# Performance work log

Measured on AMD Instinct MI355X. Metric: run time of the kernel, lower is better.

## Reference

```python
import jax, jax.numpy as jnp
import numpy as np

N_EMBD = 1024
HEAD_SIZE = 64

def setup_inputs() -> dict:
    key = jax.random.key(0)
    kx, kk, kq, kv = jax.random.split(key, 4)
    x = jax.random.normal(kx, (8, 2048, N_EMBD), dtype=jnp.float32)
    scale = 1.0 / np.sqrt(N_EMBD)
    # nn.Linear weights are [out, in]; kaiming-uniform-ish init
    Wk = jax.random.uniform(kk, (HEAD_SIZE, N_EMBD), dtype=jnp.float32, minval=-scale, maxval=scale)
    Wq = jax.random.uniform(kq, (HEAD_SIZE, N_EMBD), dtype=jnp.float32, minval=-scale, maxval=scale)
    Wv = jax.random.uniform(kv, (HEAD_SIZE, N_EMBD), dtype=jnp.float32, minval=-scale, maxval=scale)
    return {"x": x, "Wk": Wk, "Wq": Wq, "Wv": Wv}

def reference(x, Wk, Wq, Wv):
    # x: [B, T, E]; W*: [H, E] (torch Linear layout)
    k = jnp.einsum('bte,he->bth', x, Wk)
    q = jnp.einsum('bte,he->bth', x, Wq)
    v = jnp.einsum('bte,he->bth', x, Wv)
    inv_sqrt_h = 1.0 / np.sqrt(HEAD_SIZE)
    wei = jnp.einsum('bth,bsh->bts', q, k) * inv_sqrt_h  # [B, T, T]
    wei = jax.nn.softmax(wei, axis=-1)
    out = jnp.einsum('bts,bsh->bth', wei, v)  # [B, T, H]
    return out
```

## Files before the change

kernel.cpp:

```cpp
#include <hip/hip_runtime.h>
#include <cstdint>

#define NB 8
#define TS 2048
#define NE 1024
#define HD 64
#define MTOT (NB*TS)

typedef float     f4  __attribute__((ext_vector_type(4)));
typedef short     s8v __attribute__((ext_vector_type(8)));
typedef short     s4v __attribute__((ext_vector_type(4)));
typedef int       i4v __attribute__((ext_vector_type(4)));
typedef _Float16  h8  __attribute__((ext_vector_type(8)));

__device__ __forceinline__ short f2bf(float f) {
  union { float f; uint32_t u; } x; x.f = f;
  return (short)((x.u + 0x7FFFu + ((x.u >> 16) & 1u)) >> 16);
}

__device__ __forceinline__ int pack2(float lo, float hi) {
  union { float f; uint32_t u; } a, b; a.f = lo; b.f = hi;
  return (int)__builtin_amdgcn_perm(b.u + 0x8000u, a.u + 0x8000u, 0x07060302u);
}

__device__ __forceinline__ void gl2lds(const void* gptr, void* lptr) {
  auto g = (const __attribute__((address_space(1))) uint32_t*)gptr;
  auto l = (__attribute__((address_space(3))) uint32_t*)lptr;
  __builtin_amdgcn_global_load_lds(g, l, 16, 0, 0);
}

template <int N>
__device__ __forceinline__ void wait_barrier() {
  asm volatile("s_waitcnt vmcnt(%0) lgkmcnt(0)" :: "n"(N) : "memory");
  __builtin_amdgcn_s_barrier();
}

__global__ __launch_bounds__(256) void wconv_kernel(
    const float* __restrict__ Wk, const float* __restrict__ Wq, const float* __restrict__ Wv,
    short* __restrict__ wb)
{
  const int idx = (blockIdx.x * 256 + threadIdx.x) * 4;
  const int p = idx >> 16;
  const int off = idx & 65535;
  const float* W = (p == 0) ? Wq : (p == 1) ? Wk : Wv;
  const float s = (p == 0) ? 0.18033688011112042f : 1.0f;
  const float4 v = *(const float4*)&W[off];
  s4v h; h[0] = f2bf(v.x*s); h[1] = f2bf(v.y*s); h[2] = f2bf(v.z*s); h[3] = f2bf(v.w*s);
  *(s4v*)&wb[idx] = h;
}

__global__ __launch_bounds__(256) void proj_kernel(
    const float* __restrict__ x, const short* __restrict__ wb,
    short* __restrict__ qo, short* __restrict__ ko, _Float16* __restrict__ vo)
{
  __shared__ float Xs[4][32][64];
  __shared__ short Ws[2][192][64];
  const int tid = threadIdx.x;
  const int wv = tid >> 6, lane = tid & 63, n = lane & 15, quad = lane >> 4;
  const int mg = wv & 1, cg = wv >> 1;
  const int r0 = blockIdx.x * 32;
  const int xrow = lane >> 4, xslot = lane & 15;
  const int wrow = lane >> 3, wslot = lane & 7;

  auto dmaX = [&](int c, int buf) {
#pragma unroll
    for (int u = 0; u < 2; ++u) {
      const int R0 = (wv * 2 + u) * 4;
      const int row = R0 + xrow;
      const int gs = (xslot + row) & 15;
      gl2lds(&x[(size_t)(r0 + row) * NE + c * 64 + gs * 4], &Xs[buf][R0][0]);
    }
  };
  auto dmaW = [&](int c, int buf) {
#pragma unroll
    for (int u = 0; u < 6; ++u) {
      const int C0 = (wv * 6 + u) * 8;
      const int col = C0 + wrow;
      const int gs = (wslot + col) & 7;
      gl2lds(&wb[(size_t)col * NE + c * 64 + gs * 8], &Ws[buf][C0][0]);
    }
  };

  const f4 fz = {0.f, 0.f, 0.f, 0.f};
  f4 acc[6] = {fz, fz, fz, fz, fz, fz};

  auto compute = [&](int bw, int bx) {
    s8v a[2];
    const int row = mg * 16 + n;
#pragma unroll
    for (int kc = 0; kc < 2; ++kc) {
      const int u0 = kc * 8 + quad * 2;
      const float* pr = &Xs[bx][row][0];
      const f4 f0 = *(const f4*)(pr + (((u0    ) - row) & 15) * 4);
      const f4 f1 = *(const f4*)(pr + (((u0 + 1) - row) & 15) * 4);
      i4v ai;
      ai[0] = pack2(f0[0], f0[1]); ai[1] = pack2(f0[2], f0[3]);
      ai[2] = pack2(f1[0], f1[1]); ai[3] = pack2(f1[2], f1[3]);
      a[kc] = __builtin_bit_cast(s8v, ai);
    }
#pragma unroll
    for (int nf = 0; nf < 6; ++nf) {
      const int col = cg * 96 + nf * 16 + n;
      const s8v b0 = *(const s8v*)&Ws[bw][col][(((0 + quad) - col) & 7) * 8];
      const s8v b1 = *(const s8v*)&Ws[bw][col][(((4 + quad) - col) & 7) * 8];
      acc[nf] = __builtin_amdgcn_mfma_f32_16x16x32_bf16(a[0], b0, acc[nf], 0, 0, 0);
      acc[nf] = __builtin_amdgcn_mfma_f32_16x16x32_bf16(a[1], b1, acc[nf], 0, 0, 0);
    }
  };

  dmaW(0, 0); dmaX(0, 0); dmaX(1, 1); dmaX(2, 2);
  wait_barrier<4>();

  for (int t = 0; t < 16; ++t) {
    if (t <= 14) dmaW(t + 1, (t + 1) & 1);
    if (t <= 12) dmaX(t + 3, (t + 3) & 3);
    compute(t & 1, t & 3);
    if (t <= 12)      wait_barrier<2>();
    else if (t <= 14) wait_barrier<0>();
  }

#pragma unroll
  for (int nf = 0; nf < 6; ++nf) {
    const int gc = cg * 96 + nf * 16;
    const int p = gc >> 6;
    const int rcol = (gc & 63) + n;
#pragma unroll
    for (int i = 0; i < 4; ++i) {
      const int R = r0 + mg * 16 + quad * 4 + i;
      const float av = acc[nf][i];
      if (p == 0)      qo[(size_t)R * HD + rcol] = f2bf(av);
      else if (p == 1) ko[(size_t)R * HD + rcol] = f2bf(av);
      else {
        const int t2 = R & (TS - 1), b = t2 & 31;
        const int pos = (t2 & ~31) | (((b >> 2) & 3) << 3) | (((b >> 4) & 1) << 2) | (b & 3);
        vo[(size_t)(R >> 11) * HD * TS + (size_t)rcol * TS + pos] = (_Float16)av;
      }
    }
  }
}

__global__ __launch_bounds__(512) void attn_kernel(
    const short* __restrict__ q, const short* __restrict__ k,
    const _Float16* __restrict__ vT, float* __restrict__ out)
{
  __shared__ __align__(16) char smem[98304];
  const int tid = threadIdx.x;
  const int wv = tid >> 6, lane = tid & 63, n = lane & 15, quad = lane >> 4;
  const int half = wv >> 2, qw = wv & 3;
  const int batch = blockIdx.x & 7;
  const int qg = blockIdx.x >> 3;
  const int m0 = batch * TS + qg * 64;
  const short*    kb = k  + (size_t)batch * TS * HD;
  const _Float16* vb = vT + (size_t)batch * HD * TS;
  const int drow = lane >> 3, dslot = lane & 7;
  const f4 fz = {0.f, 0.f, 0.f, 0.f};

  auto kbuf = [&](int buf) { return (short*)   (smem +         (half * 3 + buf) * 8192); };
  auto vbuf = [&](int buf) { return (_Float16*)(smem + 49152 + (half * 3 + buf) * 8192); };

  auto dmaKV = [&](int tt, int buf) {
    const int c = half * 16 + tt;
#pragma unroll
    for (int u = 0; u < 2; ++u) {
      const int K0 = (qw * 2 + u) * 8;
      const int key = K0 + drow;
      const int gs = (dslot + key) & 7;
      gl2lds(&kb[(size_t)(c * 64 + key) * HD + gs * 8], kbuf(buf) + K0 * 64);
    }
#pragma unroll
    for (int u = 0; u < 2; ++u) {
      const int D0 = (qw * 2 + u) * 8;
      const int d = D0 + drow;
      const int gs = (dslot + d) & 7;
      gl2lds(&vb[(size_t)d * TS + c * 64 + gs * 8], vbuf(buf) + D0 * 64);
    }
  };

  s8v qf[2];
#pragma unroll
  for (int kc = 0; kc < 2; ++kc)
    qf[kc] = *(const s8v*)&q[(size_t)(m0 + qw * 16 + n) * HD + kc * 32 + quad * 8];

  f4 o[4] = {fz, fz, fz, fz};
  f4 lD = fz;
  h8 ones;
#pragma unroll
  for (int j = 0; j < 8; ++j) ones[j] = (_Float16)1.0f;

  dmaKV(0, 0); dmaKV(1, 1);
  wait_barrier<4>();

  for (int t = 0; t < 16; ++t) {
    const int buf = t % 3;
    if (t <= 13) dmaKV(t + 2, (t + 2) % 3);

    const short*    ks = kbuf(buf);
    const _Float16* vs = vbuf(buf);

    s8v kf[4][2];
#pragma unroll
    for (int f = 0; f < 4; ++f)
#pragma unroll
      for (int kc = 0; kc < 2; ++kc) {
        const int key = f * 16 + n;
        kf[f][kc] = *(const s8v*)&ks[key * 64 + (((kc * 4 + quad) - key) & 7) * 8];
      }

    f4 st[4];
#pragma unroll
    for (int f = 0; f < 4; ++f) {
      st[f] = __builtin_amdgcn_mfma_f32_16x16x32_bf16(kf[f][0], qf[0], fz, 0, 0, 0);
      st[f] = __builtin_amdgcn_mfma_f32_16x16x32_bf16(kf[f][1], qf[1], st[f], 0, 0, 0);
    }

    h8 pa[2];
#pragma unroll
    for (int pr = 0; pr < 2; ++pr)
#pragma unroll
      for (int hf = 0; hf < 2; ++hf)
#pragma unroll
        for (int i = 0; i < 4; ++i)
          pa[pr][hf * 4 + i] = (_Float16)__builtin_amdgcn_exp2f(st[pr * 2 + hf][i]);

#pragma unroll
    for (int pr = 0; pr < 2; ++pr) {
      lD = __builtin_amdgcn_mfma_f32_16x16x32_f16(pa[pr], ones, lD, 0, 0, 0);
#pragma unroll
      for (int g = 0; g < 4; ++g) {
        const int d = g * 16 + n;
        const h8 vf = *(const h8*)&vs[d * 64 + (((pr * 4 + quad) - d) & 7) * 8];
        o[g] = __builtin_amdgcn_mfma_f32_16x16x32_f16(pa[pr], vf, o[g], 0, 0, 0);
      }
    }

    if (t <= 13)      wait_barrier<4>();
    else if (t == 14) wait_barrier<0>();
  }

  __syncthreads();

  float* o_c = (float*)smem;
  float* l_c = (float*)(smem + 36864);
  if (n == 0)
#pragma unroll
    for (int i = 0; i < 4; ++i) l_c[wv * 16 + quad * 4 + i] = lD[i];
#pragma unroll
  for (int g = 0; g < 4; ++g)
#pragma unroll
    for (int i = 0; i < 4; ++i)
      o_c[(wv * 16 + quad * 4 + i) * 68 + g * 16 + n] = o[g][i];
  __syncthreads();

#pragma unroll
  for (int rep = 0; rep < 2; ++rep) {
    const int idx = tid + rep * 512;
    const int qr = idx >> 4, d4 = (idx & 15) * 4;
    const int qw2 = qr >> 4, wr = qr & 15;
    const float L = l_c[qw2 * 16 + wr] + l_c[(qw2 + 4) * 16 + wr];
    const f4 s0 = *(const f4*)&o_c[(qw2 * 16 + wr) * 68 + d4];
    const f4 s1 = *(const f4*)&o_c[((qw2 + 4) * 16 + wr) * 68 + d4];
    f4 r = (s0 + s1);
    const float inv = 1.0f / L;
    r[0] *= inv; r[1] *= inv; r[2] *= inv; r[3] *= inv;
    *(f4*)&out[(size_t)(m0 + qr) * HD + d4] = r;
  }
}

extern "C" void kernel_launch(void* const* d_in, const int* in_sizes, int n_in,
                              void* d_out, int out_size, void* d_ws, size_t ws_size,
                              hipStream_t stream) {
  const float* x  = (const float*)d_in[0];
  const float* Wk = (const float*)d_in[1];
  const float* Wq = (const float*)d_in[2];
  const float* Wv = (const float*)d_in[3];
  float* out = (float*)d_out;

  short* qb = (short*)d_ws;
  short* kb = qb + (size_t)MTOT * HD;
  _Float16* vb = (_Float16*)(kb + (size_t)MTOT * HD);
  short* wb = (short*)(vb + (size_t)NB * HD * TS);

  wconv_kernel<<<192, 256, 0, stream>>>(Wk, Wq, Wv, wb);
  proj_kernel<<<MTOT / 32, 256, 0, stream>>>(x, wb, qb, kb, vb);
  attn_kernel<<<MTOT / 64, 512, 0, stream>>>(qb, kb, vb, out);
}
```

Baseline: 129.5 us.

## Fuse weight conversion, projection and attention into one persistent kernel with grid barriers

Replaces three launches with one 256-block persistent kernel that converts weights, computes the QKV projection, and runs attention. The phases are separated by atomic-counter grid barriers, and a small memset resets the counters each call. Projection and attention tiling are reworked so each block covers 64 rows, using 32-key K/V tiles with a smaller LDS footprint. This removes launch gaps and inter-kernel drains but adds grid-barrier spin cost and relies on all 256 blocks being co-resident.

New measurement: 366.6 us. +183.1%, slower.

```diff
diff --git a/kernel.cpp b/kernel.cpp
--- a/kernel.cpp
+++ b/kernel.cpp
@@ -6,10 +6,10 @@
 #define NE 1024
 #define HD 64
 #define MTOT (NB*TS)
+#define NBLK 256
 
 typedef float     f4  __attribute__((ext_vector_type(4)));
 typedef short     s8v __attribute__((ext_vector_type(8)));
-typedef short     s4v __attribute__((ext_vector_type(4)));
 typedef int       i4v __attribute__((ext_vector_type(4)));
 typedef _Float16  h8  __attribute__((ext_vector_type(8)));
 
@@ -35,234 +35,230 @@
   __builtin_amdgcn_s_barrier();
 }
 
-__global__ __launch_bounds__(256) void wconv_kernel(
-    const float* __restrict__ Wk, const float* __restrict__ Wq, const float* __restrict__ Wv,
-    short* __restrict__ wb)
-{
-  const int idx = (blockIdx.x * 256 + threadIdx.x) * 4;
-  const int p = idx >> 16;
-  const int off = idx & 65535;
-  const float* W = (p == 0) ? Wq : (p == 1) ? Wk : Wv;
-  const float s = (p == 0) ? 0.18033688011112042f : 1.0f;
-  const float4 v = *(const float4*)&W[off];
-  s4v h; h[0] = f2bf(v.x*s); h[1] = f2bf(v.y*s); h[2] = f2bf(v.z*s); h[3] = f2bf(v.w*s);
-  *(s4v*)&wb[idx] = h;
-}
-
-__global__ __launch_bounds__(256) void proj_kernel(
-    const float* __restrict__ x, const short* __restrict__ wb,
-    short* __restrict__ qo, short* __restrict__ ko, _Float16* __restrict__ vo)
-{
-  __shared__ float Xs[4][32][64];
-  __shared__ short Ws[2][192][64];
-  const int tid = threadIdx.x;
-  const int wv = tid >> 6, lane = tid & 63, n = lane & 15, quad = lane >> 4;
-  const int mg = wv & 1, cg = wv >> 1;
-  const int r0 = blockIdx.x * 32;
-  const int xrow = lane >> 4, xslot = lane & 15;
-  const int wrow = lane >> 3, wslot = lane & 7;
-
-  auto dmaX = [&](int c, int buf) {
-#pragma unroll
-    for (int u = 0; u < 2; ++u) {
-      const int R0 = (wv * 2 + u) * 4;
-      const int row = R0 + xrow;
-      const int gs = (xslot + row) & 15;
-      gl2lds(&x[(size_t)(r0 + row) * NE + c * 64 + gs * 4], &Xs[buf][R0][0]);
-    }
-  };
-  auto dmaW = [&](int c, int buf) {
-#pragma unroll
-    for (int u = 0; u < 6; ++u) {
-      const int C0 = (wv * 6 + u) * 8;
-      const int col = C0 + wrow;
-      const int gs = (wslot + col) & 7;
-      gl2lds(&wb[(size_t)col * NE + c * 64 + gs * 8], &Ws[buf][C0][0]);
-    }
-  };
-
-  const f4 fz = {0.f, 0.f, 0.f, 0.f};
-  f4 acc[6] = {fz, fz, fz, fz, fz, fz};
-
-  auto compute = [&](int bw, int bx) {
-    s8v a[2];
-    const int row = mg * 16 + n;
-#pragma unroll
-    for (int kc = 0; kc < 2; ++kc) {
-      const int u0 = kc * 8 + quad * 2;
-      const float* pr = &Xs[bx][row][0];
-      const f4 f0 = *(const f4*)(pr + (((u0    ) - row) & 15) * 4);
-      const f4 f1 = *(const f4*)(pr + (((u0 + 1) - row) & 15) * 4);
-      i4v ai;
-      ai[0] = pack2(f0[0], f0[1]); ai[1] = pack2(f0[2], f0[3]);
-      ai[2] = pack2(f1[0], f1[1]); ai[3] = pack2(f1[2], f1[3]);
-      a[kc] = __builtin_bit_cast(s8v, ai);
-    }
-#pragma unroll
-    for (int nf = 0; nf < 6; ++nf) {
-      const int col = cg * 96 + nf * 16 + n;
-      const s8v b0 = *(const s8v*)&Ws[bw][col][(((0 + quad) - col) & 7) * 8];
-      const s8v b1 = *(const s8v*)&Ws[bw][col][(((4 + quad) - col) & 7) * 8];
-      acc[nf] = __builtin_amdgcn_mfma_f32_16x16x32_bf16(a[0], b0, acc[nf], 0, 0, 0);
-      acc[nf] = __builtin_amdgcn_mfma_f32_16x16x32_bf16(a[1], b1, acc[nf], 0, 0, 0);
-    }
-  };
-
-  dmaW(0, 0); dmaX(0, 0); dmaX(1, 1); dmaX(2, 2);
-  wait_barrier<4>();
-
-  for (int t = 0; t < 16; ++t) {
-    if (t <= 14) dmaW(t + 1, (t + 1) & 1);
-    if (t <= 12) dmaX(t + 3, (t + 3) & 3);
-    compute(t & 1, t & 3);
-    if (t <= 12)      wait_barrier<2>();
-    else if (t <= 14) wait_barrier<0>();
-  }
-
-#pragma unroll
-  for (int nf = 0; nf < 6; ++nf) {
-    const int gc = cg * 96 + nf * 16;
-    const int p = gc >> 6;
-    const int rcol = (gc & 63) + n;
-#pragma unroll
-    for (int i = 0; i < 4; ++i) {
-      const int R = r0 + mg * 16 + quad * 4 + i;
-      const float av = acc[nf][i];
-      if (p == 0)      qo[(size_t)R * HD + rcol] = f2bf(av);
-      else if (p == 1) ko[(size_t)R * HD + rcol] = f2bf(av);
-      else {
-        const int t2 = R & (TS - 1), b = t2 & 31;
-        const int pos = (t2 & ~31) | (((b >> 2) & 3) << 3) | (((b >> 4) & 1) << 2) | (b & 3);
-        vo[(size_t)(R >> 11) * HD * TS + (size_t)rcol * TS + pos] = (_Float16)av;
-      }
-    }
-  }
-}
-
-__global__ __launch_bounds__(512) void attn_kernel(
-    const short* __restrict__ q, const short* __restrict__ k,
-    const _Float16* __restrict__ vT, float* __restrict__ out)
+__device__ __forceinline__ void gridbar(uint32_t* cnt, int id) {
+  __threadfence();
+  __syncthreads();
+  if (threadIdx.x == 0) {
+    __hip_atomic_fetch_add(&cnt[id], 1u, __ATOMIC_RELEASE, __HIP_MEMORY_SCOPE_AGENT);
+    while (__hip_atomic_load(&cnt[id], __ATOMIC_ACQUIRE, __HIP_MEMORY_SCOPE_AGENT) < NBLK)
+      __builtin_amdgcn_s_sleep(8);
+  }
+  __syncthreads();
+  __threadfence();
+}
+
+__global__ __launch_bounds__(512, 2) void fused_kernel(
+    const float* __restrict__ x, const float* __restrict__ Wk,
+    const float* __restrict__ Wq, const float* __restrict__ Wv,
+    short* __restrict__ wb, short* __restrict__ qo, short* __restrict__ ko,
+    _Float16* __restrict__ vo, float* __restrict__ out, uint32_t* cnt)
 {
   __shared__ __align__(16) char smem[98304];
   const int tid = threadIdx.x;
   const int wv = tid >> 6, lane = tid & 63, n = lane & 15, quad = lane >> 4;
-  const int half = wv >> 2, qw = wv & 3;
-  const int batch = blockIdx.x & 7;
-  const int qg = blockIdx.x >> 3;
-  const int m0 = batch * TS + qg * 64;
-  const short*    kb = k  + (size_t)batch * TS * HD;
-  const _Float16* vb = vT + (size_t)batch * HD * TS;
-  const int drow = lane >> 3, dslot = lane & 7;
+  const int blk = blockIdx.x;
   const f4 fz = {0.f, 0.f, 0.f, 0.f};
 
-  auto kbuf = [&](int buf) { return (short*)   (smem +         (half * 3 + buf) * 8192); };
-  auto vbuf = [&](int buf) { return (_Float16*)(smem + 49152 + (half * 3 + buf) * 8192); };
-
-  auto dmaKV = [&](int tt, int buf) {
-    const int c = half * 16 + tt;
-#pragma unroll
-    for (int u = 0; u < 2; ++u) {
-      const int K0 = (qw * 2 + u) * 8;
-      const int key = K0 + drow;
-      const int gs = (dslot + key) & 7;
-      gl2lds(&kb[(size_t)(c * 64 + key) * HD + gs * 8], kbuf(buf) + K0 * 64);
+  if (blk < 192) {
+    const int idx = blk * 1024 + tid * 2;
+    const int p = idx >> 16;
+    const int off = idx & 65535;
+    const float* W = (p == 0) ? Wq : (p == 1) ? Wk : Wv;
+    const float s = (p == 0) ? 0.18033688011112042f : 1.0f;
+    const float2 v = *(const float2*)&W[off];
+    *(int*)&wb[idx] = pack2(v.x * s, v.y * s);
+  }
+  gridbar(cnt, 0);
+
+  {
+    float (*Xs)[32][64] = (float (*)[32][64])smem;
+    short (*Ws)[192][64] = (short (*)[192][64])(smem + 32768);
+    const int r0 = blk * 64;
+    const int mg = wv & 1, cg = wv >> 1;
+
+    auto dmaX = [&](int t) {
+      const int rb = r0 + ((t >> 4) << 5);
+      const int c = (t & 15) << 6;
+      const int r = (wv << 2) + (lane >> 4);
+      const int s = lane & 15;
+      gl2lds(&x[(size_t)(rb + r) * NE + c + (((s + r) & 15) << 2)], &Xs[t & 3][wv << 2][0]);
+    };
+    auto dmaW = [&](int t) {
+      const int c = (t & 15) << 6;
+#pragma unroll
+      for (int u = 0; u < 3; ++u) {
+        const int C0 = (wv * 3 + u) * 8;
+        const int col = C0 + (lane >> 3);
+        const int s = lane & 7;
+        gl2lds(&wb[(size_t)col * NE + c + (((s + col) & 7) << 3)], &Ws[t & 1][C0][0]);
+      }
+    };
+
+    f4 acc[2][3];
+#pragma unroll
+    for (int h = 0; h < 2; ++h)
+#pragma unroll
+      for (int nf = 0; nf < 3; ++nf) acc[h][nf] = fz;
+
+    dmaW(0); dmaX(0); dmaX(1); dmaX(2);
+    wait_barrier<2>();
+
+    for (int t = 0; t < 32; ++t) {
+      if (t < 31) dmaW(t + 1);
+      if (t < 29) dmaX(t + 3);
+      {
+        const int bx = t & 3, bw = t & 1;
+        const int row = (mg << 4) + n;
+        s8v a[2];
+#pragma unroll
+        for (int kc = 0; kc < 2; ++kc) {
+          const int u0 = kc * 8 + quad * 2;
+          const float* pr = &Xs[bx][row][0];
+          const f4 f0 = *(const f4*)(pr + (((u0    ) - row) & 15) * 4);
+          const f4 f1 = *(const f4*)(pr + (((u0 + 1) - row) & 15) * 4);
+          i4v ai;
+          ai[0] = pack2(f0[0], f0[1]); ai[1] = pack2(f0[2], f0[3]);
+          ai[2] = pack2(f1[0], f1[1]); ai[3] = pack2(f1[2], f1[3]);
+          a[kc] = __builtin_bit_cast(s8v, ai);
+        }
+        f4* ac = acc[t >> 4];
+#pragma unroll
+        for (int nf = 0; nf < 3; ++nf) {
+          const int col = cg * 48 + nf * 16 + n;
+          const s8v b0 = *(const s8v*)&Ws[bw][col][(((    quad) - col) & 7) * 8];
+          const s8v b1 = *(const s8v*)&Ws[bw][col][(((4 + quad) - col) & 7) * 8];
+          ac[nf] = __builtin_amdgcn_mfma_f32_16x16x32_bf16(a[0], b0, ac[nf], 0, 0, 0);
+          ac[nf] = __builtin_amdgcn_mfma_f32_16x16x32_bf16(a[1], b1, ac[nf], 0, 0, 0);
+        }
+      }
+      if (t < 29)      wait_barrier<1>();
+      else if (t < 31) wait_barrier<0>();
     }
-#pragma unroll
-    for (int u = 0; u < 2; ++u) {
-      const int D0 = (qw * 2 + u) * 8;
-      const int d = D0 + drow;
-      const int gs = (dslot + d) & 7;
-      gl2lds(&vb[(size_t)d * TS + c * 64 + gs * 8], vbuf(buf) + D0 * 64);
+
+#pragma unroll
+    for (int h = 0; h < 2; ++h)
+#pragma unroll
+      for (int nf = 0; nf < 3; ++nf) {
+        const int base = cg * 48 + nf * 16;
+        const int p = base >> 6;
+        const int rcol = (base & 63) + n;
+#pragma unroll
+        for (int i = 0; i < 4; ++i) {
+          const int R = r0 + h * 32 + mg * 16 + quad * 4 + i;
+          const float av = acc[h][nf][i];
+          if (p == 0)      qo[(size_t)R * HD + rcol] = f2bf(av);
+          else if (p == 1) ko[(size_t)R * HD + rcol] = f2bf(av);
+          else {
+            const int t2 = R & (TS - 1), b = t2 & 31;
+            const int pos = (t2 & ~31) | (((b >> 2) & 3) << 3) | (((b >> 4) & 1) << 2) | (b & 3);
+            vo[(size_t)(R >> 11) * HD * TS + (size_t)rcol * TS + pos] = (_Float16)av;
+          }
+        }
+      }
+  }
+  gridbar(cnt, 1);
+
+  {
+    const int half = wv >> 2, qw = wv & 3;
+    const int batch = blk & 7, qg = blk >> 3;
+    const int m0 = batch * TS + qg * 64;
+    const short*    kb = ko + (size_t)batch * TS * HD;
+    const _Float16* vb = vo + (size_t)batch * HD * TS;
+
+    auto kbuf = [&](int b) { return (short*)   (smem +         half * 12288 + b * 4096); };
+    auto vbuf = [&](int b) { return (_Float16*)(smem + 24576 + half * 12288 + b * 4096); };
+
+    auto dmaKV = [&](int t) {
+      const int b = t % 3;
+      const int c0 = half * 1024 + t * 32;
+      {
+        const int key = (qw << 3) + (lane >> 3);
+        const int s = lane & 7;
+        gl2lds(&kb[(size_t)(c0 + key) * HD + (((s + key) & 7) << 3)], kbuf(b) + (qw << 3) * 64);
+      }
+      {
+        const int d = (qw << 4) + (lane >> 2);
+        const int s = lane & 3;
+        gl2lds(&vb[(size_t)d * TS + c0 + (((s + d) & 3) << 3)], vbuf(b) + (qw << 4) * 32);
+      }
+    };
+
+    s8v qf[2];
+#pragma unroll
+    for (int kc = 0; kc < 2; ++kc)
+      qf[kc] = *(const s8v*)&qo[(size_t)(m0 + qw * 16 + n) * HD + kc * 32 + quad * 8];
+
+    f4 o[4] = {fz, fz, fz, fz};
+    f4 lD = fz;
+    h8 ones;
+#pragma unroll
+    for (int j = 0; j < 8; ++j) ones[j] = (_Float16)1.0f;
+
+    dmaKV(0); dmaKV(1);
+    wait_barrier<2>();
+
+    for (int t = 0; t < 32; ++t) {
+      if (t < 30) dmaKV(t + 2);
+      {
+        const short*    ks = kbuf(t % 3);
+        const _Float16* vs = vbuf(t % 3);
+        s8v kf[2][2];
+#pragma unroll
+        for (int f = 0; f < 2; ++f)
+#pragma unroll
+          for (int kc = 0; kc < 2; ++kc) {
+            const int key = f * 16 + n;
+            kf[f][kc] = *(const s8v*)&ks[key * 64 + (((kc * 4 + quad) - key) & 7) * 8];
+          }
+        f4 st[2];
+#pragma unroll
+        for (int f = 0; f < 2; ++f) {
+          st[f] = __builtin_amdgcn_mfma_f32_16x16x32_bf16(kf[f][0], qf[0], fz, 0, 0, 0);
+          st[f] = __builtin_amdgcn_mfma_f32_16x16x32_bf16(kf[f][1], qf[1], st[f], 0, 0, 0);
+        }
+        h8 pa;
+#pragma unroll
+        for (int hf = 0; hf < 2; ++hf)
+#pragma unroll
+          for (int i = 0; i < 4; ++i)
+            pa[hf * 4 + i] = (_Float16)__builtin_amdgcn_exp2f(st[hf][i]);
+
+        lD = __builtin_amdgcn_mfma_f32_16x16x32_f16(pa, ones, lD, 0, 0, 0);
+#pragma unroll
+        for (int g = 0; g < 4; ++g) {
+          const int d = g * 16 + n;
+          const h8 vf = *(const h8*)&vs[d * 32 + ((quad - d) & 3) * 8];
+          o[g] = __builtin_amdgcn_mfma_f32_16x16x32_f16(pa, vf, o[g], 0, 0, 0);
+        }
+      }
+      if (t < 30)      wait_barrier<2>();
+      else if (t < 31) wait_barrier<0>();
     }
-  };
-
-  s8v qf[2];
-#pragma unroll
-  for (int kc = 0; kc < 2; ++kc)
-    qf[kc] = *(const s8v*)&q[(size_t)(m0 + qw * 16 + n) * HD + kc * 32 + quad * 8];
-
-  f4 o[4] = {fz, fz, fz, fz};
-  f4 lD = fz;
-  h8 ones;
-#pragma unroll
-  for (int j = 0; j < 8; ++j) ones[j] = (_Float16)1.0f;
-
-  dmaKV(0, 0); dmaKV(1, 1);
-  wait_barrier<4>();
-
-  for (int t = 0; t < 16; ++t) {
-    const int buf = t % 3;
-    if (t <= 13) dmaKV(t + 2, (t + 2) % 3);
-
-    const short*    ks = kbuf(buf);
-    const _Float16* vs = vbuf(buf);
-
-    s8v kf[4][2];
-#pragma unroll
-    for (int f = 0; f < 4; ++f)
-#pragma unroll
-      for (int kc = 0; kc < 2; ++kc) {
-        const int key = f * 16 + n;
-        kf[f][kc] = *(const s8v*)&ks[key * 64 + (((kc * 4 + quad) - key) & 7) * 8];
-      }
-
-    f4 st[4];
-#pragma unroll
-    for (int f = 0; f < 4; ++f) {
-      st[f] = __builtin_amdgcn_mfma_f32_16x16x32_bf16(kf[f][0], qf[0], fz, 0, 0, 0);
-      st[f] = __builtin_amdgcn_mfma_f32_16x16x32_bf16(kf[f][1], qf[1], st[f], 0, 0, 0);
-    }
-
-    h8 pa[2];
-#pragma unroll
-    for (int pr = 0; pr < 2; ++pr)
-#pragma unroll
-      for (int hf = 0; hf < 2; ++hf)
-#pragma unroll
-        for (int i = 0; i < 4; ++i)
-          pa[pr][hf * 4 + i] = (_Float16)__builtin_amdgcn_exp2f(st[pr * 2 + hf][i]);
-
-#pragma unroll
-    for (int pr = 0; pr < 2; ++pr) {
-      lD = __builtin_amdgcn_mfma_f32_16x16x32_f16(pa[pr], ones, lD, 0, 0, 0);
-#pragma unroll
-      for (int g = 0; g < 4; ++g) {
-        const int d = g * 16 + n;
-        const h8 vf = *(const h8*)&vs[d * 64 + (((pr * 4 + quad) - d) & 7) * 8];
-        o[g] = __builtin_amdgcn_mfma_f32_16x16x32_f16(pa[pr], vf, o[g], 0, 0, 0);
-      }
-    }
-
-    if (t <= 13)      wait_barrier<4>();
-    else if (t == 14) wait_barrier<0>();
-  }
-
-  __syncthreads();
-
-  float* o_c = (float*)smem;
-  float* l_c = (float*)(smem + 36864);
-  if (n == 0)
-#pragma unroll
-    for (int i = 0; i < 4; ++i) l_c[wv * 16 + quad * 4 + i] = lD[i];
-#pragma unroll
-  for (int g = 0; g < 4; ++g)
-#pragma unroll
-    for (int i = 0; i < 4; ++i)
-      o_c[(wv * 16 + quad * 4 + i) * 68 + g * 16 + n] = o[g][i];
-  __syncthreads();
-
-#pragma unroll
-  for (int rep = 0; rep < 2; ++rep) {
-    const int idx = tid + rep * 512;
-    const int qr = idx >> 4, d4 = (idx & 15) * 4;
+
+    __syncthreads();
+    float* o_c = (float*)smem;
+    float* l_c = (float*)(smem + 34816);
+    if (n == 0)
+#pragma unroll
+      for (int i = 0; i < 4; ++i) l_c[wv * 16 + quad * 4 + i] = lD[i];
+#pragma unroll
+    for (int g = 0; g < 4; ++g)
+#pragma unroll
+      for (int i = 0; i < 4; ++i)
+        o_c[(wv * 16 + quad * 4 + i) * 68 + g * 16 + n] = o[g][i];
+    __syncthreads();
+
+    const int qr = tid >> 3, d8 = (tid & 7) * 8;
     const int qw2 = qr >> 4, wr = qr & 15;
     const float L = l_c[qw2 * 16 + wr] + l_c[(qw2 + 4) * 16 + wr];
-    const f4 s0 = *(const f4*)&o_c[(qw2 * 16 + wr) * 68 + d4];
-    const f4 s1 = *(const f4*)&o_c[((qw2 + 4) * 16 + wr) * 68 + d4];
-    f4 r = (s0 + s1);
     const float inv = 1.0f / L;
-    r[0] *= inv; r[1] *= inv; r[2] *= inv; r[3] *= inv;
-    *(f4*)&out[(size_t)(m0 + qr) * HD + d4] = r;
+    f4 s0 = *(const f4*)&o_c[(qw2 * 16 + wr) * 68 + d8];
+    f4 s1 = *(const f4*)&o_c[(qw2 * 16 + wr) * 68 + d8 + 4];
+    s0 += *(const f4*)&o_c[((qw2 + 4) * 16 + wr) * 68 + d8];
+    s1 += *(const f4*)&o_c[((qw2 + 4) * 16 + wr) * 68 + d8 + 4];
+    s0 *= inv; s1 *= inv;
+    *(f4*)&out[(size_t)(m0 + qr) * HD + d8]     = s0;
+    *(f4*)&out[(size_t)(m0 + qr) * HD + d8 + 4] = s1;
   }
 }
 
@@ -279,8 +275,8 @@
   short* kb = qb + (size_t)MTOT * HD;
   _Float16* vb = (_Float16*)(kb + (size_t)MTOT * HD);
   short* wb = (short*)(vb + (size_t)NB * HD * TS);
-
-  wconv_kernel<<<192, 256, 0, stream>>>(Wk, Wq, Wv, wb);
-  proj_kernel<<<MTOT / 32, 256, 0, stream>>>(x, wb, qb, kb, vb);
-  attn_kernel<<<MTOT / 64, 512, 0, stream>>>(qb, kb, vb, out);
-}
+  uint32_t* cnt = (uint32_t*)((char*)d_ws + (64u << 20));
+
+  hipMemsetAsync(cnt, 0, 64, stream);
+  fused_kernel<<<NBLK, 512, 0, stream>>>(x, Wk, Wq, Wv, wb, qb, kb, vb, out, cnt);
+}
```

## Halve attention block to 32 queries with four waves and double buffering

Applied to the files above, without the earlier changes.

The attention kernel now handles 32 queries per block with 256 threads (2 key halves × 2 query waves) instead of 64 queries with 512 threads, and the grid doubles. The K/V staging goes from a triple-buffered ring with partial waits to a double buffer that waits for the full copy each iteration, and each wave now loads a larger share of each tile. LDS drops from 96KB to 64KB, so two blocks may share a CU. In exchange, each K/V tile is fetched by twice as many blocks, and overlap of copies with compute is shallower.

New measurement: 131.5 us. No clear change (+1.5%).

```diff
diff --git a/kernel.cpp b/kernel.cpp
--- a/kernel.cpp
+++ b/kernel.cpp
@@ -139,40 +139,42 @@
   }
 }
 
-__global__ __launch_bounds__(512) void attn_kernel(
+__global__ __launch_bounds__(256) void attn_kernel(
     const short* __restrict__ q, const short* __restrict__ k,
     const _Float16* __restrict__ vT, float* __restrict__ out)
 {
-  __shared__ __align__(16) char smem[98304];
+  __shared__ __align__(16) char smem[65536];
   const int tid = threadIdx.x;
   const int wv = tid >> 6, lane = tid & 63, n = lane & 15, quad = lane >> 4;
-  const int half = wv >> 2, qw = wv & 3;
+  const int half = wv >> 1, qw = wv & 1;
   const int batch = blockIdx.x & 7;
   const int qg = blockIdx.x >> 3;
-  const int m0 = batch * TS + qg * 64;
+  const int m0 = batch * TS + qg * 32;
   const short*    kb = k  + (size_t)batch * TS * HD;
   const _Float16* vb = vT + (size_t)batch * HD * TS;
-  const int drow = lane >> 3, dslot = lane & 7;
   const f4 fz = {0.f, 0.f, 0.f, 0.f};
 
-  auto kbuf = [&](int buf) { return (short*)   (smem +         (half * 3 + buf) * 8192); };
-  auto vbuf = [&](int buf) { return (_Float16*)(smem + 49152 + (half * 3 + buf) * 8192); };
-
-  auto dmaKV = [&](int tt, int buf) {
-    const int c = half * 16 + tt;
-#pragma unroll
-    for (int u = 0; u < 2; ++u) {
-      const int K0 = (qw * 2 + u) * 8;
-      const int key = K0 + drow;
-      const int gs = (dslot + key) & 7;
-      gl2lds(&kb[(size_t)(c * 64 + key) * HD + gs * 8], kbuf(buf) + K0 * 64);
-    }
-#pragma unroll
-    for (int u = 0; u < 2; ++u) {
-      const int D0 = (qw * 2 + u) * 8;
-      const int d = D0 + drow;
-      const int gs = (dslot + d) & 7;
-      gl2lds(&vb[(size_t)d * TS + c * 64 + gs * 8], vbuf(buf) + D0 * 64);
+  auto kbuf = [&](int b) { return (short*)   (smem +         (half * 2 + b) * 8192); };
+  auto vbuf = [&](int b) { return (_Float16*)(smem + 32768 + (half * 2 + b) * 8192); };
+
+  auto dmaKV = [&](int t) {
+    const int b = t & 1;
+    const int c0 = half * 1024 + t * 64;
+    short*    kd = kbuf(b);
+    _Float16* vd = vbuf(b);
+#pragma unroll
+    for (int u = 0; u < 4; ++u) {
+      const int K0 = qw * 32 + u * 8;
+      const int key = K0 + (lane >> 3);
+      const int s = lane & 7;
+      gl2lds(&kb[(size_t)(c0 + key) * HD + (((s + key) & 7) << 3)], kd + K0 * 64);
+    }
+#pragma unroll
+    for (int u = 0; u < 4; ++u) {
+      const int D0 = qw * 32 + u * 8;
+      const int d = D0 + (lane >> 3);
+      const int s = lane & 7;
+      gl2lds(&vb[(size_t)d * TS + c0 + (((s + d) & 7) << 3)], vd + D0 * 64);
     }
   };
 
@@ -187,12 +189,12 @@
 #pragma unroll
   for (int j = 0; j < 8; ++j) ones[j] = (_Float16)1.0f;
 
-  dmaKV(0, 0); dmaKV(1, 1);
-  wait_barrier<4>();
+  dmaKV(0);
+  wait_barrier<0>();
 
   for (int t = 0; t < 16; ++t) {
-    const int buf = t % 3;
-    if (t <= 13) dmaKV(t + 2, (t + 2) % 3);
+    const int buf = t & 1;
+    if (t < 15) dmaKV(t + 1);
 
     const short*    ks = kbuf(buf);
     const _Float16* vs = vbuf(buf);
@@ -233,14 +235,13 @@
       }
     }
 
-    if (t <= 13)      wait_barrier<4>();
-    else if (t == 14) wait_barrier<0>();
+    if (t < 15) wait_barrier<0>();
   }
 
   __syncthreads();
 
   float* o_c = (float*)smem;
-  float* l_c = (float*)(smem + 36864);
+  float* l_c = (float*)(smem + 17408);
   if (n == 0)
 #pragma unroll
     for (int i = 0; i < 4; ++i) l_c[wv * 16 + quad * 4 + i] = lD[i];
@@ -251,19 +252,17 @@
       o_c[(wv * 16 + quad * 4 + i) * 68 + g * 16 + n] = o[g][i];
   __syncthreads();
 
-#pragma unroll
-  for (int rep = 0; rep < 2; ++rep) {
-    const int idx = tid + rep * 512;
-    const int qr = idx >> 4, d4 = (idx & 15) * 4;
-    const int qw2 = qr >> 4, wr = qr & 15;
-    const float L = l_c[qw2 * 16 + wr] + l_c[(qw2 + 4) * 16 + wr];
-    const f4 s0 = *(const f4*)&o_c[(qw2 * 16 + wr) * 68 + d4];
-    const f4 s1 = *(const f4*)&o_c[((qw2 + 4) * 16 + wr) * 68 + d4];
-    f4 r = (s0 + s1);
-    const float inv = 1.0f / L;
-    r[0] *= inv; r[1] *= inv; r[2] *= inv; r[3] *= inv;
-    *(f4*)&out[(size_t)(m0 + qr) * HD + d4] = r;
-  }
+  const int qr = tid >> 3, d8 = (tid & 7) * 8;
+  const int qw2 = qr >> 4, wr = qr & 15;
+  const float L = l_c[qw2 * 16 + wr] + l_c[(2 + qw2) * 16 + wr];
+  const float inv = 1.0f / L;
+  f4 s0 = *(const f4*)&o_c[(qw2 * 16 + wr) * 68 + d8];
+  f4 s1 = *(const f4*)&o_c[(qw2 * 16 + wr) * 68 + d8 + 4];
+  s0 += *(const f4*)&o_c[((2 + qw2) * 16 + wr) * 68 + d8];
+  s1 += *(const f4*)&o_c[((2 + qw2) * 16 + wr) * 68 + d8 + 4];
+  s0 *= inv; s1 *= inv;
+  *(f4*)&out[(size_t)(m0 + qr) * HD + d8]     = s0;
+  *(f4*)&out[(size_t)(m0 + qr) * HD + d8 + 4] = s1;
 }
 
 extern "C" void kernel_launch(void* const* d_in, const int* in_sizes, int n_in,
@@ -282,5 +281,5 @@
 
   wconv_kernel<<<192, 256, 0, stream>>>(Wk, Wq, Wv, wb);
   proj_kernel<<<MTOT / 32, 256, 0, stream>>>(x, wb, qb, kb, vb);
-  attn_kernel<<<MTOT / 64, 512, 0, stream>>>(qb, kb, vb, out);
-}
+  attn_kernel<<<MTOT / 32, 256, 0, stream>>>(qb, kb, vb, out);
+}
```

## Load projection weights directly into registers and deepen x staging pipeline

Applied to the files above, without the earlier changes.

The projection kernel no longer stages bf16 weights through LDS. Each wave now owns 48 output columns and loads its B fragments straight from global memory into registers, double-buffered across k-steps. The x tile ring grows from 4 to 6 stages with a prefetch distance of 4, and each wave covers both 16-row groups so its weight fragments are reused twice. This removes the weight LDS traffic and the matching barrier waits, at the cost of more registers and uncoalesced global weight loads that rely on L2 hits.

New measurement: 133.1 us. 1.03x slower.

```diff
diff --git a/kernel.cpp b/kernel.cpp
--- a/kernel.cpp
+++ b/kernel.cpp
@@ -53,89 +53,102 @@
     const float* __restrict__ x, const short* __restrict__ wb,
     short* __restrict__ qo, short* __restrict__ ko, _Float16* __restrict__ vo)
 {
-  __shared__ float Xs[4][32][64];
-  __shared__ short Ws[2][192][64];
+  __shared__ float Xs[6][32][64];
   const int tid = threadIdx.x;
   const int wv = tid >> 6, lane = tid & 63, n = lane & 15, quad = lane >> 4;
-  const int mg = wv & 1, cg = wv >> 1;
   const int r0 = blockIdx.x * 32;
-  const int xrow = lane >> 4, xslot = lane & 15;
-  const int wrow = lane >> 3, wslot = lane & 7;
-
-  auto dmaX = [&](int c, int buf) {
+
+  auto dmaX = [&](int c) {
 #pragma unroll
     for (int u = 0; u < 2; ++u) {
       const int R0 = (wv * 2 + u) * 4;
-      const int row = R0 + xrow;
-      const int gs = (xslot + row) & 15;
-      gl2lds(&x[(size_t)(r0 + row) * NE + c * 64 + gs * 4], &Xs[buf][R0][0]);
+      const int row = R0 + (lane >> 4);
+      const int s = lane & 15;
+      const int gs = (s + row) & 15;
+      gl2lds(&x[(size_t)(r0 + row) * NE + c * 64 + gs * 4], &Xs[c % 6][R0][0]);
     }
   };
-  auto dmaW = [&](int c, int buf) {
-#pragma unroll
-    for (int u = 0; u < 6; ++u) {
-      const int C0 = (wv * 6 + u) * 8;
-      const int col = C0 + wrow;
-      const int gs = (wslot + col) & 7;
-      gl2lds(&wb[(size_t)col * NE + c * 64 + gs * 8], &Ws[buf][C0][0]);
+  auto loadB = [&](int c, s8v (*b)[2]) {
+#pragma unroll
+    for (int nf = 0; nf < 3; ++nf) {
+      const short* wp = &wb[(size_t)(wv * 48 + nf * 16 + n) * NE + c * 64 + quad * 8];
+      b[nf][0] = *(const s8v*)wp;
+      b[nf][1] = *(const s8v*)(wp + 32);
     }
   };
 
   const f4 fz = {0.f, 0.f, 0.f, 0.f};
-  f4 acc[6] = {fz, fz, fz, fz, fz, fz};
-
-  auto compute = [&](int bw, int bx) {
-    s8v a[2];
-    const int row = mg * 16 + n;
-#pragma unroll
-    for (int kc = 0; kc < 2; ++kc) {
-      const int u0 = kc * 8 + quad * 2;
+  f4 acc[2][3];
+#pragma unroll
+  for (int m = 0; m < 2; ++m)
+#pragma unroll
+    for (int nf = 0; nf < 3; ++nf) acc[m][nf] = fz;
+
+  s8v bcur[3][2], bnxt[3][2];
+
+  loadB(0, bcur);
+  dmaX(0); dmaX(1); dmaX(2); dmaX(3);
+  wait_barrier<6>();
+
+#pragma unroll
+  for (int t = 0; t < 16; ++t) {
+    if (t < 15) loadB(t + 1, bnxt);
+    if (t < 12) dmaX(t + 4);
+
+    const int bx = t % 6;
+    s8v a[2][2];
+#pragma unroll
+    for (int m = 0; m < 2; ++m) {
+      const int row = m * 16 + n;
       const float* pr = &Xs[bx][row][0];
-      const f4 f0 = *(const f4*)(pr + (((u0    ) - row) & 15) * 4);
-      const f4 f1 = *(const f4*)(pr + (((u0 + 1) - row) & 15) * 4);
-      i4v ai;
-      ai[0] = pack2(f0[0], f0[1]); ai[1] = pack2(f0[2], f0[3]);
-      ai[2] = pack2(f1[0], f1[1]); ai[3] = pack2(f1[2], f1[3]);
-      a[kc] = __builtin_bit_cast(s8v, ai);
-    }
-#pragma unroll
-    for (int nf = 0; nf < 6; ++nf) {
-      const int col = cg * 96 + nf * 16 + n;
-      const s8v b0 = *(const s8v*)&Ws[bw][col][(((0 + quad) - col) & 7) * 8];
-      const s8v b1 = *(const s8v*)&Ws[bw][col][(((4 + quad) - col) & 7) * 8];
-      acc[nf] = __builtin_amdgcn_mfma_f32_16x16x32_bf16(a[0], b0, acc[nf], 0, 0, 0);
-      acc[nf] = __builtin_amdgcn_mfma_f32_16x16x32_bf16(a[1], b1, acc[nf], 0, 0, 0);
-    }
-  };
-
-  dmaW(0, 0); dmaX(0, 0); dmaX(1, 1); dmaX(2, 2);
-  wait_barrier<4>();
-
-  for (int t = 0; t < 16; ++t) {
-    if (t <= 14) dmaW(t + 1, (t + 1) & 1);
-    if (t <= 12) dmaX(t + 3, (t + 3) & 3);
-    compute(t & 1, t & 3);
-    if (t <= 12)      wait_barrier<2>();
-    else if (t <= 14) wait_barrier<0>();
-  }
-
-#pragma unroll
-  for (int nf = 0; nf < 6; ++nf) {
-    const int gc = cg * 96 + nf * 16;
-    const int p = gc >> 6;
-    const int rcol = (gc & 63) + n;
-#pragma unroll
-    for (int i = 0; i < 4; ++i) {
-      const int R = r0 + mg * 16 + quad * 4 + i;
-      const float av = acc[nf][i];
-      if (p == 0)      qo[(size_t)R * HD + rcol] = f2bf(av);
-      else if (p == 1) ko[(size_t)R * HD + rcol] = f2bf(av);
-      else {
-        const int t2 = R & (TS - 1), b = t2 & 31;
-        const int pos = (t2 & ~31) | (((b >> 2) & 3) << 3) | (((b >> 4) & 1) << 2) | (b & 3);
-        vo[(size_t)(R >> 11) * HD * TS + (size_t)rcol * TS + pos] = (_Float16)av;
-      }
-    }
+#pragma unroll
+      for (int kc = 0; kc < 2; ++kc) {
+        const int u0 = kc * 8 + quad * 2;
+        const f4 f0 = *(const f4*)(pr + (((u0    ) - row) & 15) * 4);
+        const f4 f1 = *(const f4*)(pr + (((u0 + 1) - row) & 15) * 4);
+        i4v ai;
+        ai[0] = pack2(f0[0], f0[1]); ai[1] = pack2(f0[2], f0[3]);
+        ai[2] = pack2(f1[0], f1[1]); ai[3] = pack2(f1[2], f1[3]);
+        a[m][kc] = __builtin_bit_cast(s8v, ai);
+      }
+    }
+#pragma unroll
+    for (int nf = 0; nf < 3; ++nf)
+#pragma unroll
+      for (int m = 0; m < 2; ++m) {
+        acc[m][nf] = __builtin_amdgcn_mfma_f32_16x16x32_bf16(a[m][0], bcur[nf][0], acc[m][nf], 0, 0, 0);
+        acc[m][nf] = __builtin_amdgcn_mfma_f32_16x16x32_bf16(a[m][1], bcur[nf][1], acc[m][nf], 0, 0, 0);
+      }
+#pragma unroll
+    for (int nf = 0; nf < 3; ++nf)
+#pragma unroll
+      for (int kc = 0; kc < 2; ++kc) bcur[nf][kc] = bnxt[nf][kc];
+
+    if (t < 12)       wait_barrier<10>();
+    else if (t == 12) wait_barrier<8>();
+    else if (t == 13) wait_barrier<6>();
+    else if (t == 14) wait_barrier<6>();
+  }
+
+#pragma unroll
+  for (int nf = 0; nf < 3; ++nf) {
+    const int base = wv * 48 + nf * 16;
+    const int p = base >> 6;
+    const int rcol = (base & 63) + n;
+#pragma unroll
+    for (int m = 0; m < 2; ++m)
+#pragma unroll
+      for (int i = 0; i < 4; ++i) {
+        const int R = r0 + m * 16 + quad * 4 + i;
+        const float av = acc[m][nf][i];
+        if (p == 0)      qo[(size_t)R * HD + rcol] = f2bf(av);
+        else if (p == 1) ko[(size_t)R * HD + rcol] = f2bf(av);
+        else {
+          const int t2 = R & (TS - 1), b = t2 & 31;
+          const int pos = (t2 & ~31) | (((b >> 2) & 3) << 3) | (((b >> 4) & 1) << 2) | (b & 3);
+          vo[(size_t)(R >> 11) * HD * TS + (size_t)rcol * TS + pos] = (_Float16)av;
+        }
+      }
   }
 }
 
@@ -259,7 +272,7 @@
     const float L = l_c[qw2 * 16 + wr] + l_c[(qw2 + 4) * 16 + wr];
     const f4 s0 = *(const f4*)&o_c[(qw2 * 16 + wr) * 68 + d4];
     const f4 s1 = *(const f4*)&o_c[((qw2 + 4) * 16 + wr) * 68 + d4];
-    f4 r = (s0 + s1);
+    f4 r = s0 + s1;
     const float inv = 1.0f / L;
     r[0] *= inv; r[1] *= inv; r[2] *= inv; r[3] *= inv;
     *(f4*)&out[(size_t)(m0 + qr) * HD + d4] = r;
```
